# Kernel optimization log

Measured on AMD Instinct MI355X. Metric: run time of the kernel, lower is better.

Reference implementation:

```python
import jax, jax.numpy as jnp
import numpy as np

MUL = 32          # multiplicity of 0e and 1o in node/edge/out irreps
SQRT3 = np.sqrt(3.0).astype(np.float32)


def _split(x, mul):
    # x: [E, mul + mul*3] laid out as [mul x 0e | mul x 1o]
    s = x[:, :mul]
    v = x[:, mul:].reshape(x.shape[0], mul, 3)
    return s, v


def _mlp(x, W1, W2, W3):
    # e3nn-style FullyConnectedNet: no bias, 1/sqrt(fan_in) scaling, silu between layers
    h = jax.nn.silu(x @ (W1 / np.sqrt(np.float32(W1.shape[0]))))
    h = jax.nn.silu(h @ (W2 / np.sqrt(np.float32(W2.shape[0]))))
    return h @ (W3 / np.sqrt(np.float32(W3.shape[0])))


def _tp(s1, v1, s2, v2, W1, W2, W3, W4):
    # 'uvw' tensor product with irreps2 = 1x0e+1x1o (mul2 = 1).
    # CG paths: 0e*0e->0e, 0e*1o->1o, 1o*0e->1o, 1o*1o->0e (dot/sqrt(3)).
    alpha = 1.0 / np.sqrt(np.float32(s1.shape[1]))  # path norm 1/sqrt(mul1*mul2)
    out0a = jnp.einsum('uw,eu->ew', W1, s1 * s2[:, None]) * alpha
    out1a = jnp.einsum('uw,eu,em->ewm', W2, s1, v2) * alpha
    out1b = jnp.einsum('uw,eum->ewm', W3, v1 * s2[:, None, None]) * alpha
    dot = jnp.einsum('eum,em->eu', v1, v2) / SQRT3
    out0b = jnp.einsum('uw,eu->ew', W4, dot) * alpha
    # mid irreps (sorted+simplified): [2*MUL x 0e | 2*MUL x 1o]
    return jnp.concatenate([out0a, out0b], 1), jnp.concatenate([out1a, out1b], 1)


def _lin_scale(ms, mv, w):
    # LinearScaleWithWeights: per-edge generated weights, block per irrep
    E, U = ms.shape
    ws = w[:, :U * MUL].reshape(E, U, MUL)
    wv = w[:, U * MUL:].reshape(E, U, MUL)
    a = 1.0 / np.sqrt(np.float32(U))
    return (jnp.einsum('eu,euw->ew', ms, ws) * a,
            jnp.einsum('eum,euw->ewm', mv, wv) * a)


def _lin_out(s, v, Ls, Lv):
    # o3.Linear with internal shared weights, block-diagonal per irrep
    a = 1.0 / np.sqrt(np.float32(MUL))
    return s @ Ls * a, jnp.einsum('eum,uw->ewm', v, Lv) * a


def reference(node_feats_src, node_feats_dst, edge_feats, local_env_edge, edge_scalars,
              Wn_tp1, Wn_tp2, Wn_tp3, Wn_tp4, We_tp1, We_tp2, We_tp3, We_tp4,
              Wn_mlp1, Wn_mlp2, Wn_mlp3, We_mlp1, We_mlp2, We_mlp3,
              Lns, Lnv, Les, Lev):
    ss, sv = _split(node_feats_src, MUL)
    ds, dv = _split(node_feats_dst, MUL)
    # AttentionHeadsToVector over stacked (src, dst): concat heads along mul axis
    ns = jnp.concatenate([ss, ds], 1)     # [E, 64] (64x0e)
    nv = jnp.concatenate([sv, dv], 1)     # [E, 64, 3] (64x1o)
    es, ev = _split(edge_feats, MUL)
    ls = local_env_edge[:, 0]             # 1x0e
    lv = local_env_edge[:, 1:4]           # 1x1o
    # node branch
    wn = _mlp(edge_scalars, Wn_mlp1, Wn_mlp2, Wn_mlp3)   # [E, 4096]
    ms, mv = _tp(ns, nv, ls, lv, Wn_tp1, Wn_tp2, Wn_tp3, Wn_tp4)
    n_s, n_v = _lin_scale(ms, mv, wn)
    n_s, n_v = _lin_out(n_s, n_v, Lns, Lnv)
    # edge branch
    we = _mlp(edge_scalars, We_mlp1, We_mlp2, We_mlp3)   # [E, 4096]
    ms2, mv2 = _tp(es, ev, ls, lv, We_tp1, We_tp2, We_tp3, We_tp4)
    e_s, e_v = _lin_scale(ms2, mv2, we)
    e_s, e_v = _lin_out(e_s, e_v, Les, Lev)
    out_s = n_s + e_s
    out_v = n_v + e_v
    return jnp.concatenate([out_s, out_v.reshape(out_v.shape[0], -1)], 1)  # [E, 128]


def setup_inputs() -> dict:
    key = jax.random.key(0)
    ks = jax.random.split(key, 23)
    E = 30000
    rn = lambda k, shape: jax.random.normal(k, shape, dtype=jnp.float32)
    return {
        'node_feats_src': rn(ks[0], (E, 128)),
        'node_feats_dst': rn(ks[1], (E, 128)),
        'edge_feats': rn(ks[2], (E, 128)),
        'local_env_edge': rn(ks[3], (E, 4)),
        'edge_scalars': rn(ks[4], (E, 8)),
        'Wn_tp1': rn(ks[5], (64, 32)), 'Wn_tp2': rn(ks[6], (64, 32)),
        'Wn_tp3': rn(ks[7], (64, 32)), 'Wn_tp4': rn(ks[8], (64, 32)),
        'We_tp1': rn(ks[9], (32, 32)), 'We_tp2': rn(ks[10], (32, 32)),
        'We_tp3': rn(ks[11], (32, 32)), 'We_tp4': rn(ks[12], (32, 32)),
        'Wn_mlp1': rn(ks[13], (8, 64)), 'Wn_mlp2': rn(ks[14], (64, 64)),
        'Wn_mlp3': rn(ks[15], (64, 4096)),
        'We_mlp1': rn(ks[16], (8, 64)), 'We_mlp2': rn(ks[17], (64, 64)),
        'We_mlp3': rn(ks[18], (64, 4096)),
        'Lns': rn(ks[19], (32, 32)), 'Lnv': rn(ks[20], (32, 32)),
        'Les': rn(ks[21], (32, 32)), 'Lev': rn(ks[22], (32, 32)),
    }
```

## Files before the change

### kernel.cpp

```cpp
#include <hip/hip_runtime.h>

typedef __attribute__((ext_vector_type(8))) __bf16 bf16x8;
typedef __attribute__((ext_vector_type(4))) float f32x4;

#define MFMA16(A,B,C) __builtin_amdgcn_mfma_f32_16x16x32_bf16(A,B,C,0,0,0)

typedef const __attribute__((address_space(1))) void* gas_ptr;
typedef __attribute__((address_space(3))) void* las_ptr;

#define BARRIER() do { asm volatile("" ::: "memory"); __builtin_amdgcn_s_barrier(); asm volatile("" ::: "memory"); } while (0)
#define WAIT_VM4() asm volatile("s_waitcnt vmcnt(4)" ::: "memory")
#define WAIT_VM0() asm volatile("s_waitcnt vmcnt(0)" ::: "memory")

#define WS_W3N 0
#define WS_W3E 262144
#define WS_TN  524288
#define WS_TE  532480
#define WS_M1N 536576
#define WS_M2N 538624
#define WS_M1E 542720
#define WS_M2E 544768
#define WS_CNT 548864

__global__ void prep_kernel(
    const float* __restrict__ Wn1, const float* __restrict__ Wn2,
    const float* __restrict__ Wn3, const float* __restrict__ Wn4,
    const float* __restrict__ We1, const float* __restrict__ We2,
    const float* __restrict__ We3, const float* __restrict__ We4,
    const float* __restrict__ Mn1, const float* __restrict__ Mn2, const float* __restrict__ Mn3,
    const float* __restrict__ Me1, const float* __restrict__ Me2, const float* __restrict__ Me3,
    const float* __restrict__ Lns, const float* __restrict__ Lnv,
    const float* __restrict__ Les, const float* __restrict__ Lev,
    __bf16* __restrict__ ws)
{
  int idx = blockIdx.x * 256 + threadIdx.x;
  const float c1 = 0.0027621359f;
  const float an = 0.125f;
  const float ae = 0.17677669529663687f;
  const float r3 = 0.5773502691896258f;
  const float m1s = 0.35355339059327373f;
  const float m2s = 0.125f;
  if (idx < 524288) {
    int br = idx >> 18;
    int rem = idx & 262143;
    int j = rem >> 12;
    int kc = rem & 4095;
    int vh = kc >> 11;
    int r2 = kc & 2047;
    int u = r2 >> 5, wp = r2 & 31;
    const float* M3 = br ? Me3 : Mn3;
    const float* L  = vh ? (br ? Lev : Lnv) : (br ? Les : Lns);
    const float* mrow = M3 + (size_t)j * 4096 + vh * 2048 + u * 32;
    float s = 0.f;
    #pragma unroll
    for (int w = 0; w < 32; ++w) s += mrow[w] * L[w * 32 + wp];
    ws[(br ? WS_W3E : WS_W3N) + (size_t)kc * 64 + j] = (__bf16)(s * c1);
  } else if (idx < 524288 + 8192) {
    int t = idx - 524288;
    int i = t >> 11; int r = t & 2047; int w = r >> 6; int u = r & 63;
    const float* W = (i == 0) ? Wn1 : (i == 1) ? Wn2 : (i == 2) ? Wn3 : Wn4;
    float sc = an * ((i == 3) ? r3 : 1.f);
    ws[WS_TN + t] = (__bf16)(W[u * 32 + w] * sc);
  } else if (idx < 524288 + 12288) {
    int t = idx - 532480;
    int i = t >> 10; int r = t & 1023; int w = r >> 5; int u = r & 31;
    const float* W = (i == 0) ? We1 : (i == 1) ? We2 : (i == 2) ? We3 : We4;
    float sc = ae * ((i == 3) ? r3 : 1.f);
    ws[WS_TE + t] = (__bf16)(W[u * 32 + w] * sc);
  } else if (idx < 536576 + 2048) {
    int t = idx - 536576;
    int j = t >> 5, k = t & 31;
    ws[WS_M1N + t] = (__bf16)((k < 8) ? Mn1[k * 64 + j] * m1s : 0.f);
  } else if (idx < 538624 + 4096) {
    int t = idx - 538624;
    int j2 = t >> 6, j = t & 63;
    ws[WS_M2N + t] = (__bf16)(Mn2[j * 64 + j2] * m2s);
  } else if (idx < 542720 + 2048) {
    int t = idx - 542720;
    int j = t >> 5, k = t & 31;
    ws[WS_M1E + t] = (__bf16)((k < 8) ? Me1[k * 64 + j] * m1s : 0.f);
  } else if (idx < 544768 + 4096) {
    int t = idx - 544768;
    int j2 = t >> 6, j = t & 63;
    ws[WS_M2E + t] = (__bf16)(Me2[j * 64 + j2] * m2s);
  }
}

__device__ __forceinline__ float siluf(float x) { return x / (1.0f + __expf(-x)); }
__device__ __forceinline__ unsigned int pk2(float lo, float hi) {
  unsigned short a = __builtin_bit_cast(unsigned short, (__bf16)lo);
  unsigned short b = __builtin_bit_cast(unsigned short, (__bf16)hi);
  return (unsigned int)a | ((unsigned int)b << 16);
}
__device__ __forceinline__ float bflo(unsigned int v) { return __builtin_bit_cast(float, (unsigned int)(v << 16)); }
__device__ __forceinline__ float bfhi(unsigned int v) { return __builtin_bit_cast(float, (unsigned int)(v & 0xffff0000u)); }

__global__ __launch_bounds__(256, 2) void fused_kernel(
    const float* __restrict__ nsrc, const float* __restrict__ ndst,
    const float* __restrict__ efeat, const float* __restrict__ lenv,
    const float* __restrict__ escal,
    const __bf16* __restrict__ ws,
    float* __restrict__ out, int E)
{
  __shared__ __align__(16) char lds[81920];
  const int tid = threadIdx.x;
  const int wave = tid >> 6, l = tid & 63;
  const int lg = l >> 4, li = l & 15;
  const int ebase = blockIdx.x * 64;

  char* coeff = lds;
  char* afpriv = lds + 32768 + wave * 12288;
  char* h2n = lds + 32768;
  char* h2e = lds + 32768 + 8192;

  const int uh  = wave >> 1;
  const int rtw = wave & 1;

  auto stage = [&](int buf, int branch, int b) {
    const char* gbase = (const char*)(ws + (branch ? WS_W3E : WS_W3N));
    int u = uh * 32 + b;
    char* dst = afpriv + buf * 4096 + l * 16;
    int srow = rtw * 16 + (l >> 3);
    int scol = ((l & 7) ^ (l >> 3)) << 4;
    const char* src = gbase + (size_t)u * 4096 + srow * 128 + scol;
    #pragma unroll
    for (int r = 0; r < 4; ++r) {
      int gv = r >> 1, j = r & 1;
      __builtin_amdgcn_global_load_lds((gas_ptr)(src + gv * 262144 + j * 1024),
                                       (las_ptr)(dst + gv * 2048 + j * 1024), 16, 0, 0);
    }
  };

  {
    const int br = wave >> 1;
    const __bf16* M1 = ws + (br ? WS_M1E : WS_M1N);
    const __bf16* M2 = ws + (br ? WS_M2E : WS_M2N);
    char* h2buf = br ? h2e : h2n;
    char* h1s = lds + wave * 8192;
    #pragma unroll 1
    for (int c2 = 0; c2 < 2; ++c2) {
      int ct = (wave & 1) * 2 + c2;
      int el = ct * 16 + li;
      int hl = c2 * 16 + li;
      int ee = min(ebase + el, E - 1);
      bf16x8 bx;
      #pragma unroll
      for (int i = 0; i < 8; ++i) bx[i] = (__bf16)0.f;
      if (lg == 0) {
        const float* xp = escal + (size_t)ee * 8;
        float4 t0 = *(const float4*)(xp);
        float4 t1 = *(const float4*)(xp + 4);
        bx[0]=(__bf16)t0.x; bx[1]=(__bf16)t0.y; bx[2]=(__bf16)t0.z; bx[3]=(__bf16)t0.w;
        bx[4]=(__bf16)t1.x; bx[5]=(__bf16)t1.y; bx[6]=(__bf16)t1.z; bx[7]=(__bf16)t1.w;
      }
      f32x4 hc[4];
      #pragma unroll
      for (int rt = 0; rt < 4; ++rt) {
        bf16x8 a = *(const bf16x8*)(M1 + (rt * 16 + li) * 32 + lg * 8);
        f32x4 c = {0.f, 0.f, 0.f, 0.f};
        hc[rt] = MFMA16(a, bx, c);
      }
      #pragma unroll
      for (int rt = 0; rt < 4; ++rt) {
        int j0 = rt * 16 + lg * 4;
        int g = j0 >> 3;
        int addr = hl * 128 + (((g ^ (hl & 7)) << 4)) + (j0 & 7) * 2;
        uint2 wv; wv.x = pk2(siluf(hc[rt][0]), siluf(hc[rt][1]));
        wv.y = pk2(siluf(hc[rt][2]), siluf(hc[rt][3]));
        *(uint2*)(h1s + addr) = wv;
      }
      f32x4 h2c[4];
      #pragma unroll
      for (int rt = 0; rt < 4; ++rt) { f32x4 z = {0.f,0.f,0.f,0.f}; h2c[rt] = z; }
      #pragma unroll
      for (int kj = 0; kj < 2; ++kj) {
        bf16x8 b = *(const bf16x8*)(h1s + hl * 128 + (((kj * 4 + lg) ^ (hl & 7)) << 4));
        #pragma unroll
        for (int rt = 0; rt < 4; ++rt) {
          bf16x8 a = *(const bf16x8*)(M2 + (rt * 16 + li) * 64 + kj * 32 + lg * 8);
          h2c[rt] = MFMA16(a, b, h2c[rt]);
        }
      }
      #pragma unroll
      for (int rt = 0; rt < 4; ++rt) {
        int j0 = rt * 16 + lg * 4;
        int g = j0 >> 3;
        int addr = el * 128 + (((g ^ (el & 7)) << 4)) + (j0 & 7) * 2;
        uint2 wv; wv.x = pk2(siluf(h2c[rt][0]), siluf(h2c[rt][1]));
        wv.y = pk2(siluf(h2c[rt][2]), siluf(h2c[rt][3]));
        *(uint2*)(h2buf + addr) = wv;
      }
    }
  }
  __syncthreads();

  bf16x8 bbN[4][2], bbE[4][2];
  #pragma unroll
  for (int ct = 0; ct < 4; ++ct)
    #pragma unroll
    for (int kj = 0; kj < 2; ++kj) {
      int el = ct * 16 + li;
      int off = el * 128 + (((kj * 4 + lg) ^ (el & 7)) << 4);
      bbN[ct][kj] = *(const bf16x8*)(h2n + off);
      bbE[ct][kj] = *(const bf16x8*)(h2e + off);
    }
  __syncthreads();

  auto q_phase = [&](const float* f0, const float* f1, int nk, const __bf16* T, int ustride) {
    #pragma unroll 1
    for (int ct = 0; ct < 4; ++ct) {
      int el = ct * 16 + li;
      int ee = min(ebase + el, E - 1);
      const float4 le = *(const float4*)(lenv + (size_t)ee * 4);
      const size_t erow = (size_t)ee * 128;
      if (uh == 0) {
        f32x4 q1c = {0.f,0.f,0.f,0.f}, q2c = {0.f,0.f,0.f,0.f};
        for (int kj = 0; kj < nk; ++kj) {
          const float* fp = (kj ? f1 : f0) + erow + lg * 8;
          float4 t0 = *(const float4*)(fp);
          float4 t1 = *(const float4*)(fp + 4);
          bf16x8 b;
          b[0]=(__bf16)t0.x; b[1]=(__bf16)t0.y; b[2]=(__bf16)t0.z; b[3]=(__bf16)t0.w;
          b[4]=(__bf16)t1.x; b[5]=(__bf16)t1.y; b[6]=(__bf16)t1.z; b[7]=(__bf16)t1.w;
          bf16x8 a1 = *(const bf16x8*)(T + (rtw * 16 + li) * ustride + kj * 32 + lg * 8);
          bf16x8 a2 = *(const bf16x8*)(T + 32 * ustride + (rtw * 16 + li) * ustride + kj * 32 + lg * 8);
          q1c = MFMA16(a1, b, q1c);
          q2c = MFMA16(a2, b, q2c);
        }
        #pragma unroll
        for (int r = 0; r < 4; ++r) {
          uint2 cw;
          cw.x = pk2(q1c[r] * le.x, q2c[r] * le.y);
          cw.y = pk2(q2c[r] * le.z, q2c[r] * le.w);
          *(uint2*)(coeff + (rtw * 16 + lg * 4 + r) * 512 + el * 8) = cw;
        }
      } else {
        f32x4 q30 = {0.f,0.f,0.f,0.f}, q31 = {0.f,0.f,0.f,0.f}, q32 = {0.f,0.f,0.f,0.f}, q4c = {0.f,0.f,0.f,0.f};
        for (int kj = 0; kj < nk; ++kj) {
          const float* fp = (kj ? f1 : f0) + erow + 32 + lg * 24;
          float v[24];
          #pragma unroll
          for (int q = 0; q < 6; ++q) {
            float4 t = *(const float4*)(fp + q * 4);
            v[q*4] = t.x; v[q*4+1] = t.y; v[q*4+2] = t.z; v[q*4+3] = t.w;
          }
          bf16x8 b0, b1, b2, bd;
          #pragma unroll
          for (int i = 0; i < 8; ++i) {
            b0[i] = (__bf16)v[3*i]; b1[i] = (__bf16)v[3*i+1]; b2[i] = (__bf16)v[3*i+2];
            bd[i] = (__bf16)(v[3*i] * le.y + v[3*i+1] * le.z + v[3*i+2] * le.w);
          }
          bf16x8 a3 = *(const bf16x8*)(T + 2 * 32 * ustride + (rtw * 16 + li) * ustride + kj * 32 + lg * 8);
          bf16x8 a4 = *(const bf16x8*)(T + 3 * 32 * ustride + (rtw * 16 + li) * ustride + kj * 32 + lg * 8);
          q30 = MFMA16(a3, b0, q30); q31 = MFMA16(a3, b1, q31); q32 = MFMA16(a3, b2, q32);
          q4c = MFMA16(a4, bd, q4c);
        }
        #pragma unroll
        for (int r = 0; r < 4; ++r) {
          uint2 cw;
          cw.x = pk2(q4c[r], q30[r] * le.x);
          cw.y = pk2(q31[r] * le.x, q32[r] * le.x);
          *(uint2*)(coeff + (32 + rtw * 16 + lg * 4 + r) * 512 + el * 8) = cw;
        }
      }
    }
  };

  f32x4 aS[4], aV[4][3];
  #pragma unroll
  for (int ct = 0; ct < 4; ++ct) {
    f32x4 z = {0.f,0.f,0.f,0.f};
    aS[ct] = z; aV[ct][0] = z; aV[ct][1] = z; aV[ct][2] = z;
  }

  auto main_block = [&](int buf, int b, const bf16x8 (&bb)[4][2]) {
    const char* afb = afpriv + buf * 4096;
    int u_rel = uh * 32 + b;
    bf16x8 afS[2], afV[2];
    #pragma unroll
    for (int kj = 0; kj < 2; ++kj) {
      int off = li * 128 + (((kj * 4 + lg) ^ (li & 7)) << 4);
      afS[kj] = *(const bf16x8*)(afb + off);
      afV[kj] = *(const bf16x8*)(afb + 2048 + off);
    }
    #pragma unroll
    for (int ct = 0; ct < 4; ++ct) {
      uint2 cf = *(const uint2*)(coeff + u_rel * 512 + (ct * 16 + li) * 8);
      float ms = bflo(cf.x), m0 = bfhi(cf.x), m1 = bflo(cf.y), m2 = bfhi(cf.y);
      f32x4 c = {0.f,0.f,0.f,0.f};
      c = MFMA16(afS[0], bb[ct][0], c);
      c = MFMA16(afS[1], bb[ct][1], c);
      aS[ct] += ms * c;
      f32x4 d = {0.f,0.f,0.f,0.f};
      d = MFMA16(afV[0], bb[ct][0], d);
      d = MFMA16(afV[1], bb[ct][1], d);
      aV[ct][0] += m0 * d;
      aV[ct][1] += m1 * d;
      aV[ct][2] += m2 * d;
    }
  };

  stage(0, 0, 0);
  stage(1, 0, 1);
  q_phase(nsrc, ndst, 2, ws + WS_TN, 64);
  __syncthreads();

  #pragma unroll 1
  for (int b = 0; b < 32; ++b) {
    if (b < 30) stage((b + 2) % 3, 0, b + 2);
    else        stage((b + 2) % 3, 1, b - 30);
    main_block(b % 3, b, bbN);
    WAIT_VM4();
  }
  BARRIER();

  q_phase(efeat, efeat, 1, ws + WS_TE, 32);
  __syncthreads();

  #pragma unroll 1
  for (int b = 0; b < 32; ++b) {
    if (b < 30) stage((b + 4) % 3, 1, b + 2);
    main_block((b + 2) % 3, b, bbE);
    if (b == 30) { WAIT_VM0(); }
    else         { WAIT_VM4(); }
  }
  BARRIER();

  char* R1 = lds;
  auto rmw = [&](bool add) {
    #pragma unroll
    for (int ct = 0; ct < 4; ++ct) {
      int e = ct * 16 + li;
      char* epp = R1 + e * 512;
      f32x4 s = aS[ct];
      char* p = epp + (((rtw * 4 + lg) ^ (e & 7)) << 4);
      if (add) s += *(const f32x4*)p;
      *(f32x4*)p = s;
      #pragma unroll
      for (int m = 0; m < 3; ++m) {
        f32x4 x = aV[ct][m];
        char* q = epp + (((8 + m * 8 + rtw * 4 + lg) ^ (e & 7)) << 4);
        if (add) x += *(const f32x4*)q;
        *(f32x4*)q = x;
      }
    }
  };
  if (uh == 0) rmw(false);
  __syncthreads();
  if (uh == 1) rmw(true);
  __syncthreads();

  #pragma unroll
  for (int it = 0; it < 8; ++it) {
    int chunk = it * 256 + tid;
    int e = chunk >> 5, c4 = chunk & 31;
    f32x4 v;
    #pragma unroll
    for (int q = 0; q < 4; ++q) {
      int f = c4 * 4 + q;
      int g, wd;
      if (f < 32) { g = f >> 2; wd = f & 3; }
      else { int t = f - 32; int w = t / 3; int m = t - w * 3; g = 8 + m * 8 + (w >> 2); wd = w & 3; }
      v[q] = *(const float*)(R1 + e * 512 + ((g ^ (e & 7)) << 4) + wd * 4);
    }
    int ge = ebase + e;
    if (ge < E) *(f32x4*)(out + (size_t)ge * 128 + c4 * 4) = v;
  }
}

extern "C" void kernel_launch(void* const* d_in, const int* in_sizes, int n_in,
                              void* d_out, int out_size, void* d_ws, size_t ws_size,
                              hipStream_t stream) {
  const float* nsrc  = (const float*)d_in[0];
  const float* ndst  = (const float*)d_in[1];
  const float* efeat = (const float*)d_in[2];
  const float* lenv  = (const float*)d_in[3];
  const float* escal = (const float*)d_in[4];
  const float* Wn1 = (const float*)d_in[5];
  const float* Wn2 = (const float*)d_in[6];
  const float* Wn3 = (const float*)d_in[7];
  const float* Wn4 = (const float*)d_in[8];
  const float* We1 = (const float*)d_in[9];
  const float* We2 = (const float*)d_in[10];
  const float* We3 = (const float*)d_in[11];
  const float* We4 = (const float*)d_in[12];
  const float* Mn1 = (const float*)d_in[13];
  const float* Mn2 = (const float*)d_in[14];
  const float* Mn3 = (const float*)d_in[15];
  const float* Me1 = (const float*)d_in[16];
  const float* Me2 = (const float*)d_in[17];
  const float* Me3 = (const float*)d_in[18];
  const float* Lns = (const float*)d_in[19];
  const float* Lnv = (const float*)d_in[20];
  const float* Les = (const float*)d_in[21];
  const float* Lev = (const float*)d_in[22];
  (void)n_in; (void)ws_size;

  int E = in_sizes[0] / 128;
  __bf16* ws = (__bf16*)d_ws;
  float* outp = (float*)d_out;
  (void)out_size;

  int nprep = (WS_CNT + 255) / 256;
  hipLaunchKernelGGL(prep_kernel, dim3(nprep), dim3(256), 0, stream,
                     Wn1, Wn2, Wn3, Wn4, We1, We2, We3, We4,
                     Mn1, Mn2, Mn3, Me1, Me2, Me3,
                     Lns, Lnv, Les, Lev, ws);

  int nwg = (E + 63) / 64;
  hipLaunchKernelGGL(fused_kernel, dim3(nwg), dim3(256), 0, stream,
                     nsrc, ndst, efeat, lenv, escal, ws, outp, E);
}
```

Before: 75.95 us.

## Split node and edge branches into separate workgroups combined by atomic adds

```diff
diff --git a/kernel.cpp b/kernel.cpp
--- a/kernel.cpp
+++ b/kernel.cpp
@@ -9,7 +9,6 @@
 typedef __attribute__((address_space(3))) void* las_ptr;
 
 #define BARRIER() do { asm volatile("" ::: "memory"); __builtin_amdgcn_s_barrier(); asm volatile("" ::: "memory"); } while (0)
-#define WAIT_VM4() asm volatile("s_waitcnt vmcnt(4)" ::: "memory")
 #define WAIT_VM0() asm volatile("s_waitcnt vmcnt(0)" ::: "memory")
 
 #define WS_W3N 0
@@ -102,107 +101,100 @@
     const __bf16* __restrict__ ws,
     float* __restrict__ out, int E)
 {
-  __shared__ __align__(16) char lds[81920];
+  __shared__ __align__(16) char lds[57344];
   const int tid = threadIdx.x;
   const int wave = tid >> 6, l = tid & 63;
   const int lg = l >> 4, li = l & 15;
-  const int ebase = blockIdx.x * 64;
+  const int br = blockIdx.x & 1;
+  const int ebase = (blockIdx.x >> 1) * 64;
 
   char* coeff = lds;
-  char* afpriv = lds + 32768 + wave * 12288;
-  char* h2n = lds + 32768;
-  char* h2e = lds + 32768 + 8192;
-
-  const int uh  = wave >> 1;
+  char* afbase = lds + 32768;
+  char* h2buf = afbase;
+
+  const int ep  = wave >> 1;
   const int rtw = wave & 1;
-
-  auto stage = [&](int buf, int branch, int b) {
-    const char* gbase = (const char*)(ws + (branch ? WS_W3E : WS_W3N));
-    int u = uh * 32 + b;
-    char* dst = afpriv + buf * 4096 + l * 16;
-    int srow = rtw * 16 + (l >> 3);
-    int scol = ((l & 7) ^ (l >> 3)) << 4;
-    const char* src = gbase + (size_t)u * 4096 + srow * 128 + scol;
-    #pragma unroll
-    for (int r = 0; r < 4; ++r) {
-      int gv = r >> 1, j = r & 1;
-      __builtin_amdgcn_global_load_lds((gas_ptr)(src + gv * 262144 + j * 1024),
-                                       (las_ptr)(dst + gv * 2048 + j * 1024), 16, 0, 0);
+  const int qh  = wave >> 1;
+  const int qr  = wave & 1;
+
+  const char* gbase = (const char*)(ws + (br ? WS_W3E : WS_W3N));
+
+  auto stage = [&](int buf, int u) {
+    int row = tid >> 3, col = tid & 7;
+    int roff = row * 128 + (((col ^ (row & 7))) << 4);
+    char* dst = afbase + buf * 8192 + tid * 16;
+    #pragma unroll
+    for (int r = 0; r < 2; ++r) {
+      const char* src = gbase + r * 262144 + (size_t)u * 4096 + roff;
+      __builtin_amdgcn_global_load_lds((gas_ptr)src, (las_ptr)(dst + r * 4096), 16, 0, 0);
     }
   };
 
   {
-    const int br = wave >> 1;
     const __bf16* M1 = ws + (br ? WS_M1E : WS_M1N);
     const __bf16* M2 = ws + (br ? WS_M2E : WS_M2N);
-    char* h2buf = br ? h2e : h2n;
     char* h1s = lds + wave * 8192;
-    #pragma unroll 1
-    for (int c2 = 0; c2 < 2; ++c2) {
-      int ct = (wave & 1) * 2 + c2;
-      int el = ct * 16 + li;
-      int hl = c2 * 16 + li;
-      int ee = min(ebase + el, E - 1);
-      bf16x8 bx;
-      #pragma unroll
-      for (int i = 0; i < 8; ++i) bx[i] = (__bf16)0.f;
-      if (lg == 0) {
-        const float* xp = escal + (size_t)ee * 8;
-        float4 t0 = *(const float4*)(xp);
-        float4 t1 = *(const float4*)(xp + 4);
-        bx[0]=(__bf16)t0.x; bx[1]=(__bf16)t0.y; bx[2]=(__bf16)t0.z; bx[3]=(__bf16)t0.w;
-        bx[4]=(__bf16)t1.x; bx[5]=(__bf16)t1.y; bx[6]=(__bf16)t1.z; bx[7]=(__bf16)t1.w;
-      }
-      f32x4 hc[4];
+    int el = wave * 16 + li;
+    int hl = li;
+    int ee = min(ebase + el, E - 1);
+    bf16x8 bx;
+    #pragma unroll
+    for (int i = 0; i < 8; ++i) bx[i] = (__bf16)0.f;
+    if (lg == 0) {
+      const float* xp = escal + (size_t)ee * 8;
+      float4 t0 = *(const float4*)(xp);
+      float4 t1 = *(const float4*)(xp + 4);
+      bx[0]=(__bf16)t0.x; bx[1]=(__bf16)t0.y; bx[2]=(__bf16)t0.z; bx[3]=(__bf16)t0.w;
+      bx[4]=(__bf16)t1.x; bx[5]=(__bf16)t1.y; bx[6]=(__bf16)t1.z; bx[7]=(__bf16)t1.w;
+    }
+    f32x4 hc[4];
+    #pragma unroll
+    for (int rt = 0; rt < 4; ++rt) {
+      bf16x8 a = *(const bf16x8*)(M1 + (rt * 16 + li) * 32 + lg * 8);
+      f32x4 c = {0.f, 0.f, 0.f, 0.f};
+      hc[rt] = MFMA16(a, bx, c);
+    }
+    #pragma unroll
+    for (int rt = 0; rt < 4; ++rt) {
+      int j0 = rt * 16 + lg * 4;
+      int g = j0 >> 3;
+      int addr = hl * 128 + (((g ^ (hl & 7)) << 4)) + (j0 & 7) * 2;
+      uint2 wv; wv.x = pk2(siluf(hc[rt][0]), siluf(hc[rt][1]));
+      wv.y = pk2(siluf(hc[rt][2]), siluf(hc[rt][3]));
+      *(uint2*)(h1s + addr) = wv;
+    }
+    f32x4 h2c[4];
+    #pragma unroll
+    for (int rt = 0; rt < 4; ++rt) { f32x4 z = {0.f,0.f,0.f,0.f}; h2c[rt] = z; }
+    #pragma unroll
+    for (int kj = 0; kj < 2; ++kj) {
+      bf16x8 b = *(const bf16x8*)(h1s + hl * 128 + (((kj * 4 + lg) ^ (hl & 7)) << 4));
       #pragma unroll
       for (int rt = 0; rt < 4; ++rt) {
-        bf16x8 a = *(const bf16x8*)(M1 + (rt * 16 + li) * 32 + lg * 8);
-        f32x4 c = {0.f, 0.f, 0.f, 0.f};
-        hc[rt] = MFMA16(a, bx, c);
+        bf16x8 a = *(const bf16x8*)(M2 + (rt * 16 + li) * 64 + kj * 32 + lg * 8);
+        h2c[rt] = MFMA16(a, b, h2c[rt]);
       }
-      #pragma unroll
-      for (int rt = 0; rt < 4; ++rt) {
-        int j0 = rt * 16 + lg * 4;
-        int g = j0 >> 3;
-        int addr = hl * 128 + (((g ^ (hl & 7)) << 4)) + (j0 & 7) * 2;
-        uint2 wv; wv.x = pk2(siluf(hc[rt][0]), siluf(hc[rt][1]));
-        wv.y = pk2(siluf(hc[rt][2]), siluf(hc[rt][3]));
-        *(uint2*)(h1s + addr) = wv;
-      }
-      f32x4 h2c[4];
-      #pragma unroll
-      for (int rt = 0; rt < 4; ++rt) { f32x4 z = {0.f,0.f,0.f,0.f}; h2c[rt] = z; }
-      #pragma unroll
-      for (int kj = 0; kj < 2; ++kj) {
-        bf16x8 b = *(const bf16x8*)(h1s + hl * 128 + (((kj * 4 + lg) ^ (hl & 7)) << 4));
-        #pragma unroll
-        for (int rt = 0; rt < 4; ++rt) {
-          bf16x8 a = *(const bf16x8*)(M2 + (rt * 16 + li) * 64 + kj * 32 + lg * 8);
-          h2c[rt] = MFMA16(a, b, h2c[rt]);
-        }
-      }
-      #pragma unroll
-      for (int rt = 0; rt < 4; ++rt) {
-        int j0 = rt * 16 + lg * 4;
-        int g = j0 >> 3;
-        int addr = el * 128 + (((g ^ (el & 7)) << 4)) + (j0 & 7) * 2;
-        uint2 wv; wv.x = pk2(siluf(h2c[rt][0]), siluf(h2c[rt][1]));
-        wv.y = pk2(siluf(h2c[rt][2]), siluf(h2c[rt][3]));
-        *(uint2*)(h2buf + addr) = wv;
-      }
+    }
+    #pragma unroll
+    for (int rt = 0; rt < 4; ++rt) {
+      int j0 = rt * 16 + lg * 4;
+      int g = j0 >> 3;
+      int addr = el * 128 + (((g ^ (el & 7)) << 4)) + (j0 & 7) * 2;
+      uint2 wv; wv.x = pk2(siluf(h2c[rt][0]), siluf(h2c[rt][1]));
+      wv.y = pk2(siluf(h2c[rt][2]), siluf(h2c[rt][3]));
+      *(uint2*)(h2buf + addr) = wv;
     }
   }
   __syncthreads();
 
-  bf16x8 bbN[4][2], bbE[4][2];
+  bf16x8 bb[2][2];
   #pragma unroll
-  for (int ct = 0; ct < 4; ++ct)
+  for (int ct2 = 0; ct2 < 2; ++ct2)
     #pragma unroll
     for (int kj = 0; kj < 2; ++kj) {
-      int el = ct * 16 + li;
+      int el = ep * 32 + ct2 * 16 + li;
       int off = el * 128 + (((kj * 4 + lg) ^ (el & 7)) << 4);
-      bbN[ct][kj] = *(const bf16x8*)(h2n + off);
-      bbE[ct][kj] = *(const bf16x8*)(h2e + off);
+      bb[ct2][kj] = *(const bf16x8*)(h2buf + off);
     }
   __syncthreads();
 
@@ -213,7 +205,7 @@
       int ee = min(ebase + el, E - 1);
       const float4 le = *(const float4*)(lenv + (size_t)ee * 4);
       const size_t erow = (size_t)ee * 128;
-      if (uh == 0) {
+      if (qh == 0) {
         f32x4 q1c = {0.f,0.f,0.f,0.f}, q2c = {0.f,0.f,0.f,0.f};
         for (int kj = 0; kj < nk; ++kj) {
           const float* fp = (kj ? f1 : f0) + erow + lg * 8;
@@ -222,8 +214,8 @@
           bf16x8 b;
           b[0]=(__bf16)t0.x; b[1]=(__bf16)t0.y; b[2]=(__bf16)t0.z; b[3]=(__bf16)t0.w;
           b[4]=(__bf16)t1.x; b[5]=(__bf16)t1.y; b[6]=(__bf16)t1.z; b[7]=(__bf16)t1.w;
-          bf16x8 a1 = *(const bf16x8*)(T + (rtw * 16 + li) * ustride + kj * 32 + lg * 8);
-          bf16x8 a2 = *(const bf16x8*)(T + 32 * ustride + (rtw * 16 + li) * ustride + kj * 32 + lg * 8);
+          bf16x8 a1 = *(const bf16x8*)(T + (qr * 16 + li) * ustride + kj * 32 + lg * 8);
+          bf16x8 a2 = *(const bf16x8*)(T + 32 * ustride + (qr * 16 + li) * ustride + kj * 32 + lg * 8);
           q1c = MFMA16(a1, b, q1c);
           q2c = MFMA16(a2, b, q2c);
         }
@@ -232,7 +224,7 @@
           uint2 cw;
           cw.x = pk2(q1c[r] * le.x, q2c[r] * le.y);
           cw.y = pk2(q2c[r] * le.z, q2c[r] * le.w);
-          *(uint2*)(coeff + (rtw * 16 + lg * 4 + r) * 512 + el * 8) = cw;
+          *(uint2*)(coeff + (qr * 16 + lg * 4 + r) * 512 + el * 8) = cw;
         }
       } else {
         f32x4 q30 = {0.f,0.f,0.f,0.f}, q31 = {0.f,0.f,0.f,0.f}, q32 = {0.f,0.f,0.f,0.f}, q4c = {0.f,0.f,0.f,0.f};
@@ -250,8 +242,8 @@
             b0[i] = (__bf16)v[3*i]; b1[i] = (__bf16)v[3*i+1]; b2[i] = (__bf16)v[3*i+2];
             bd[i] = (__bf16)(v[3*i] * le.y + v[3*i+1] * le.z + v[3*i+2] * le.w);
           }
-          bf16x8 a3 = *(const bf16x8*)(T + 2 * 32 * ustride + (rtw * 16 + li) * ustride + kj * 32 + lg * 8);
-          bf16x8 a4 = *(const bf16x8*)(T + 3 * 32 * ustride + (rtw * 16 + li) * ustride + kj * 32 + lg * 8);
+          bf16x8 a3 = *(const bf16x8*)(T + 2 * 32 * ustride + (qr * 16 + li) * ustride + kj * 32 + lg * 8);
+          bf16x8 a4 = *(const bf16x8*)(T + 3 * 32 * ustride + (qr * 16 + li) * ustride + kj * 32 + lg * 8);
           q30 = MFMA16(a3, b0, q30); q31 = MFMA16(a3, b1, q31); q32 = MFMA16(a3, b2, q32);
           q4c = MFMA16(a4, bd, q4c);
         }
@@ -260,94 +252,71 @@
           uint2 cw;
           cw.x = pk2(q4c[r], q30[r] * le.x);
           cw.y = pk2(q31[r] * le.x, q32[r] * le.x);
-          *(uint2*)(coeff + (32 + rtw * 16 + lg * 4 + r) * 512 + el * 8) = cw;
+          *(uint2*)(coeff + (32 + qr * 16 + lg * 4 + r) * 512 + el * 8) = cw;
         }
       }
     }
   };
 
-  f32x4 aS[4], aV[4][3];
+  f32x4 aS[2], aV[2][3];
   #pragma unroll
-  for (int ct = 0; ct < 4; ++ct) {
+  for (int ct2 = 0; ct2 < 2; ++ct2) {
     f32x4 z = {0.f,0.f,0.f,0.f};
-    aS[ct] = z; aV[ct][0] = z; aV[ct][1] = z; aV[ct][2] = z;
-  }
-
-  auto main_block = [&](int buf, int b, const bf16x8 (&bb)[4][2]) {
-    const char* afb = afpriv + buf * 4096;
-    int u_rel = uh * 32 + b;
+    aS[ct2] = z; aV[ct2][0] = z; aV[ct2][1] = z; aV[ct2][2] = z;
+  }
+
+  auto main_block = [&](int buf, int u) {
+    const char* afb = afbase + buf * 8192;
     bf16x8 afS[2], afV[2];
     #pragma unroll
     for (int kj = 0; kj < 2; ++kj) {
-      int off = li * 128 + (((kj * 4 + lg) ^ (li & 7)) << 4);
+      int off = (rtw * 16 + li) * 128 + (((kj * 4 + lg) ^ (li & 7)) << 4);
       afS[kj] = *(const bf16x8*)(afb + off);
-      afV[kj] = *(const bf16x8*)(afb + 2048 + off);
-    }
-    #pragma unroll
-    for (int ct = 0; ct < 4; ++ct) {
-      uint2 cf = *(const uint2*)(coeff + u_rel * 512 + (ct * 16 + li) * 8);
+      afV[kj] = *(const bf16x8*)(afb + 4096 + off);
+    }
+    #pragma unroll
+    for (int ct2 = 0; ct2 < 2; ++ct2) {
+      int e = ep * 32 + ct2 * 16 + li;
+      uint2 cf = *(const uint2*)(coeff + u * 512 + e * 8);
       float ms = bflo(cf.x), m0 = bfhi(cf.x), m1 = bflo(cf.y), m2 = bfhi(cf.y);
       f32x4 c = {0.f,0.f,0.f,0.f};
-      c = MFMA16(afS[0], bb[ct][0], c);
-      c = MFMA16(afS[1], bb[ct][1], c);
-      aS[ct] += ms * c;
+      c = MFMA16(afS[0], bb[ct2][0], c);
+      c = MFMA16(afS[1], bb[ct2][1], c);
+      aS[ct2] += ms * c;
       f32x4 d = {0.f,0.f,0.f,0.f};
-      d = MFMA16(afV[0], bb[ct][0], d);
-      d = MFMA16(afV[1], bb[ct][1], d);
-      aV[ct][0] += m0 * d;
-      aV[ct][1] += m1 * d;
-      aV[ct][2] += m2 * d;
+      d = MFMA16(afV[0], bb[ct2][0], d);
+      d = MFMA16(afV[1], bb[ct2][1], d);
+      aV[ct2][0] += m0 * d;
+      aV[ct2][1] += m1 * d;
+      aV[ct2][2] += m2 * d;
     }
   };
 
-  stage(0, 0, 0);
-  stage(1, 0, 1);
-  q_phase(nsrc, ndst, 2, ws + WS_TN, 64);
+  stage(0, 0);
+  stage(1, 1);
+  if (br == 0) q_phase(nsrc, ndst, 2, ws + WS_TN, 64);
+  else         q_phase(efeat, efeat, 1, ws + WS_TE, 32);
   __syncthreads();
 
   #pragma unroll 1
-  for (int b = 0; b < 32; ++b) {
-    if (b < 30) stage((b + 2) % 3, 0, b + 2);
-    else        stage((b + 2) % 3, 1, b - 30);
-    main_block(b % 3, b, bbN);
-    WAIT_VM4();
-  }
-  BARRIER();
-
-  q_phase(efeat, efeat, 1, ws + WS_TE, 32);
-  __syncthreads();
-
-  #pragma unroll 1
-  for (int b = 0; b < 32; ++b) {
-    if (b < 30) stage((b + 4) % 3, 1, b + 2);
-    main_block((b + 2) % 3, b, bbE);
-    if (b == 30) { WAIT_VM0(); }
-    else         { WAIT_VM4(); }
-  }
-  BARRIER();
+  for (int b = 0; b < 64; ++b) {
+    if (b < 62) stage((b + 2) % 3, b + 2);
+    main_block(b % 3, b);
+    WAIT_VM0();
+    BARRIER();
+  }
 
   char* R1 = lds;
-  auto rmw = [&](bool add) {
-    #pragma unroll
-    for (int ct = 0; ct < 4; ++ct) {
-      int e = ct * 16 + li;
-      char* epp = R1 + e * 512;
-      f32x4 s = aS[ct];
-      char* p = epp + (((rtw * 4 + lg) ^ (e & 7)) << 4);
-      if (add) s += *(const f32x4*)p;
-      *(f32x4*)p = s;
-      #pragma unroll
-      for (int m = 0; m < 3; ++m) {
-        f32x4 x = aV[ct][m];
-        char* q = epp + (((8 + m * 8 + rtw * 4 + lg) ^ (e & 7)) << 4);
-        if (add) x += *(const f32x4*)q;
-        *(f32x4*)q = x;
-      }
-    }
-  };
-  if (uh == 0) rmw(false);
-  __syncthreads();
-  if (uh == 1) rmw(true);
+  #pragma unroll
+  for (int ct2 = 0; ct2 < 2; ++ct2) {
+    int e = ep * 32 + ct2 * 16 + li;
+    char* epp = R1 + e * 512;
+    f32x4 s = aS[ct2];
+    *(f32x4*)(epp + (((rtw * 4 + lg) ^ (e & 7)) << 4)) = s;
+    #pragma unroll
+    for (int m = 0; m < 3; ++m)
+      *(f32x4*)(epp + (((8 + m * 8 + rtw * 4 + lg) ^ (e & 7)) << 4)) = aV[ct2][m];
+  }
   __syncthreads();
 
   #pragma unroll
@@ -364,7 +333,13 @@
       v[q] = *(const float*)(R1 + e * 512 + ((g ^ (e & 7)) << 4) + wd * 4);
     }
     int ge = ebase + e;
-    if (ge < E) *(f32x4*)(out + (size_t)ge * 128 + c4 * 4) = v;
+    if (ge < E) {
+      float* dst = out + (size_t)ge * 128 + c4 * 4;
+      atomicAdd(dst + 0, v[0]);
+      atomicAdd(dst + 1, v[1]);
+      atomicAdd(dst + 2, v[2]);
+      atomicAdd(dst + 3, v[3]);
+    }
   }
 }
 
@@ -399,7 +374,8 @@
   int E = in_sizes[0] / 128;
   __bf16* ws = (__bf16*)d_ws;
   float* outp = (float*)d_out;
-  (void)out_size;
+
+  hipMemsetAsync(d_out, 0, (size_t)out_size * sizeof(float), stream);
 
   int nprep = (WS_CNT + 255) / 256;
   hipLaunchKernelGGL(prep_kernel, dim3(nprep), dim3(256), 0, stream,
@@ -407,7 +383,7 @@
                      Mn1, Mn2, Mn3, Me1, Me2, Me3,
                      Lns, Lnv, Les, Lev, ws);
 
-  int nwg = (E + 63) / 64;
-  hipLaunchKernelGGL(fused_kernel, dim3(nwg), dim3(256), 0, stream,
+  int ngroups = (E + 63) / 64;
+  hipLaunchKernelGGL(fused_kernel, dim3(ngroups * 2), dim3(256), 0, stream,
                      nsrc, ndst, efeat, lenv, escal, ws, outp, E);
 }
```

Measured after the change: 172.6 us. 127% more time.

## Halve edges per block, share staged weights across waves, double-buffer with barriers

Applied to the files above, without the earlier changes.

```diff
diff --git a/kernel.cpp b/kernel.cpp
--- a/kernel.cpp
+++ b/kernel.cpp
@@ -7,10 +7,6 @@
 
 typedef const __attribute__((address_space(1))) void* gas_ptr;
 typedef __attribute__((address_space(3))) void* las_ptr;
-
-#define BARRIER() do { asm volatile("" ::: "memory"); __builtin_amdgcn_s_barrier(); asm volatile("" ::: "memory"); } while (0)
-#define WAIT_VM4() asm volatile("s_waitcnt vmcnt(4)" ::: "memory")
-#define WAIT_VM0() asm volatile("s_waitcnt vmcnt(0)" ::: "memory")
 
 #define WS_W3N 0
 #define WS_W3E 262144
@@ -95,120 +91,115 @@
 __device__ __forceinline__ float bflo(unsigned int v) { return __builtin_bit_cast(float, (unsigned int)(v << 16)); }
 __device__ __forceinline__ float bfhi(unsigned int v) { return __builtin_bit_cast(float, (unsigned int)(v & 0xffff0000u)); }
 
-__global__ __launch_bounds__(256, 2) void fused_kernel(
+__global__ __launch_bounds__(256, 3) void fused_kernel(
     const float* __restrict__ nsrc, const float* __restrict__ ndst,
     const float* __restrict__ efeat, const float* __restrict__ lenv,
     const float* __restrict__ escal,
     const __bf16* __restrict__ ws,
     float* __restrict__ out, int E)
 {
-  __shared__ __align__(16) char lds[81920];
+  __shared__ __align__(16) char lds[49152];
   const int tid = threadIdx.x;
   const int wave = tid >> 6, l = tid & 63;
   const int lg = l >> 4, li = l & 15;
-  const int ebase = blockIdx.x * 64;
+  const int ebase = blockIdx.x * 32;
 
   char* coeff = lds;
-  char* afpriv = lds + 32768 + wave * 12288;
-  char* h2n = lds + 32768;
-  char* h2e = lds + 32768 + 8192;
+  char* afbase = lds + 16384;
+  char* h2n = afbase;
+  char* h2e = afbase + 4096;
 
   const int uh  = wave >> 1;
   const int rtw = wave & 1;
 
   auto stage = [&](int buf, int branch, int b) {
     const char* gbase = (const char*)(ws + (branch ? WS_W3E : WS_W3N));
-    int u = uh * 32 + b;
-    char* dst = afpriv + buf * 4096 + l * 16;
-    int srow = rtw * 16 + (l >> 3);
-    int scol = ((l & 7) ^ (l >> 3)) << 4;
-    const char* src = gbase + (size_t)u * 4096 + srow * 128 + scol;
+    char* dst = afbase + buf * 16384 + tid * 16;
+    int row = tid >> 3, col = tid & 7;
+    int roff = row * 128 + ((col ^ (row & 7)) << 4);
     #pragma unroll
     for (int r = 0; r < 4; ++r) {
-      int gv = r >> 1, j = r & 1;
-      __builtin_amdgcn_global_load_lds((gas_ptr)(src + gv * 262144 + j * 1024),
-                                       (las_ptr)(dst + gv * 2048 + j * 1024), 16, 0, 0);
+      int u = b + (r >> 1) * 32, gv = r & 1;
+      const char* src = gbase + gv * 262144 + u * 4096 + roff;
+      __builtin_amdgcn_global_load_lds((gas_ptr)src, (las_ptr)(dst + r * 4096), 16, 0, 0);
     }
   };
 
   {
     const int br = wave >> 1;
+    const int ct = wave & 1;
     const __bf16* M1 = ws + (br ? WS_M1E : WS_M1N);
     const __bf16* M2 = ws + (br ? WS_M2E : WS_M2N);
     char* h2buf = br ? h2e : h2n;
-    char* h1s = lds + wave * 8192;
-    #pragma unroll 1
-    for (int c2 = 0; c2 < 2; ++c2) {
-      int ct = (wave & 1) * 2 + c2;
-      int el = ct * 16 + li;
-      int hl = c2 * 16 + li;
-      int ee = min(ebase + el, E - 1);
-      bf16x8 bx;
-      #pragma unroll
-      for (int i = 0; i < 8; ++i) bx[i] = (__bf16)0.f;
-      if (lg == 0) {
-        const float* xp = escal + (size_t)ee * 8;
-        float4 t0 = *(const float4*)(xp);
-        float4 t1 = *(const float4*)(xp + 4);
-        bx[0]=(__bf16)t0.x; bx[1]=(__bf16)t0.y; bx[2]=(__bf16)t0.z; bx[3]=(__bf16)t0.w;
-        bx[4]=(__bf16)t1.x; bx[5]=(__bf16)t1.y; bx[6]=(__bf16)t1.z; bx[7]=(__bf16)t1.w;
-      }
-      f32x4 hc[4];
+    char* h1s = lds + wave * 4096;
+    int el = ct * 16 + li;
+    int hl = li;
+    int ee = min(ebase + el, E - 1);
+    bf16x8 bx;
+    #pragma unroll
+    for (int i = 0; i < 8; ++i) bx[i] = (__bf16)0.f;
+    if (lg == 0) {
+      const float* xp = escal + (size_t)ee * 8;
+      float4 t0 = *(const float4*)(xp);
+      float4 t1 = *(const float4*)(xp + 4);
+      bx[0]=(__bf16)t0.x; bx[1]=(__bf16)t0.y; bx[2]=(__bf16)t0.z; bx[3]=(__bf16)t0.w;
+      bx[4]=(__bf16)t1.x; bx[5]=(__bf16)t1.y; bx[6]=(__bf16)t1.z; bx[7]=(__bf16)t1.w;
+    }
+    f32x4 hc[4];
+    #pragma unroll
+    for (int rt = 0; rt < 4; ++rt) {
+      bf16x8 a = *(const bf16x8*)(M1 + (rt * 16 + li) * 32 + lg * 8);
+      f32x4 c = {0.f, 0.f, 0.f, 0.f};
+      hc[rt] = MFMA16(a, bx, c);
+    }
+    #pragma unroll
+    for (int rt = 0; rt < 4; ++rt) {
+      int j0 = rt * 16 + lg * 4;
+      int g = j0 >> 3;
+      int addr = hl * 128 + (((g ^ (hl & 7)) << 4)) + (j0 & 7) * 2;
+      uint2 wv; wv.x = pk2(siluf(hc[rt][0]), siluf(hc[rt][1]));
+      wv.y = pk2(siluf(hc[rt][2]), siluf(hc[rt][3]));
+      *(uint2*)(h1s + addr) = wv;
+    }
+    f32x4 h2c[4];
+    #pragma unroll
+    for (int rt = 0; rt < 4; ++rt) { f32x4 z = {0.f,0.f,0.f,0.f}; h2c[rt] = z; }
+    #pragma unroll
+    for (int kj = 0; kj < 2; ++kj) {
+      bf16x8 b = *(const bf16x8*)(h1s + hl * 128 + (((kj * 4 + lg) ^ (hl & 7)) << 4));
       #pragma unroll
       for (int rt = 0; rt < 4; ++rt) {
-        bf16x8 a = *(const bf16x8*)(M1 + (rt * 16 + li) * 32 + lg * 8);
-        f32x4 c = {0.f, 0.f, 0.f, 0.f};
-        hc[rt] = MFMA16(a, bx, c);
+        bf16x8 a = *(const bf16x8*)(M2 + (rt * 16 + li) * 64 + kj * 32 + lg * 8);
+        h2c[rt] = MFMA16(a, b, h2c[rt]);
       }
-      #pragma unroll
-      for (int rt = 0; rt < 4; ++rt) {
-        int j0 = rt * 16 + lg * 4;
-        int g = j0 >> 3;
-        int addr = hl * 128 + (((g ^ (hl & 7)) << 4)) + (j0 & 7) * 2;
-        uint2 wv; wv.x = pk2(siluf(hc[rt][0]), siluf(hc[rt][1]));
-        wv.y = pk2(siluf(hc[rt][2]), siluf(hc[rt][3]));
-        *(uint2*)(h1s + addr) = wv;
-      }
-      f32x4 h2c[4];
-      #pragma unroll
-      for (int rt = 0; rt < 4; ++rt) { f32x4 z = {0.f,0.f,0.f,0.f}; h2c[rt] = z; }
-      #pragma unroll
-      for (int kj = 0; kj < 2; ++kj) {
-        bf16x8 b = *(const bf16x8*)(h1s + hl * 128 + (((kj * 4 + lg) ^ (hl & 7)) << 4));
-        #pragma unroll
-        for (int rt = 0; rt < 4; ++rt) {
-          bf16x8 a = *(const bf16x8*)(M2 + (rt * 16 + li) * 64 + kj * 32 + lg * 8);
-          h2c[rt] = MFMA16(a, b, h2c[rt]);
-        }
-      }
-      #pragma unroll
-      for (int rt = 0; rt < 4; ++rt) {
-        int j0 = rt * 16 + lg * 4;
-        int g = j0 >> 3;
-        int addr = el * 128 + (((g ^ (el & 7)) << 4)) + (j0 & 7) * 2;
-        uint2 wv; wv.x = pk2(siluf(h2c[rt][0]), siluf(h2c[rt][1]));
-        wv.y = pk2(siluf(h2c[rt][2]), siluf(h2c[rt][3]));
-        *(uint2*)(h2buf + addr) = wv;
-      }
-    }
-  }
-  __syncthreads();
-
-  bf16x8 bbN[4][2], bbE[4][2];
+    }
+    #pragma unroll
+    for (int rt = 0; rt < 4; ++rt) {
+      int j0 = rt * 16 + lg * 4;
+      int g = j0 >> 3;
+      int addr = el * 128 + (((g ^ (el & 7)) << 4)) + (j0 & 7) * 2;
+      uint2 wv; wv.x = pk2(siluf(h2c[rt][0]), siluf(h2c[rt][1]));
+      wv.y = pk2(siluf(h2c[rt][2]), siluf(h2c[rt][3]));
+      *(uint2*)(h2buf + addr) = wv;
+    }
+  }
+  __syncthreads();
+
+  bf16x8 bbN[2][2], bbE[2][2];
   #pragma unroll
-  for (int ct = 0; ct < 4; ++ct)
+  for (int ct2 = 0; ct2 < 2; ++ct2)
     #pragma unroll
     for (int kj = 0; kj < 2; ++kj) {
-      int el = ct * 16 + li;
+      int el = ct2 * 16 + li;
       int off = el * 128 + (((kj * 4 + lg) ^ (el & 7)) << 4);
-      bbN[ct][kj] = *(const bf16x8*)(h2n + off);
-      bbE[ct][kj] = *(const bf16x8*)(h2e + off);
+      bbN[ct2][kj] = *(const bf16x8*)(h2n + off);
+      bbE[ct2][kj] = *(const bf16x8*)(h2e + off);
     }
   __syncthreads();
 
   auto q_phase = [&](const float* f0, const float* f1, int nk, const __bf16* T, int ustride) {
     #pragma unroll 1
-    for (int ct = 0; ct < 4; ++ct) {
+    for (int ct = 0; ct < 2; ++ct) {
       int el = ct * 16 + li;
       int ee = min(ebase + el, E - 1);
       const float4 le = *(const float4*)(lenv + (size_t)ee * 4);
@@ -232,7 +223,7 @@
           uint2 cw;
           cw.x = pk2(q1c[r] * le.x, q2c[r] * le.y);
           cw.y = pk2(q2c[r] * le.z, q2c[r] * le.w);
-          *(uint2*)(coeff + (rtw * 16 + lg * 4 + r) * 512 + el * 8) = cw;
+          *(uint2*)(coeff + (rtw * 16 + lg * 4 + r) * 256 + el * 8) = cw;
         }
       } else {
         f32x4 q30 = {0.f,0.f,0.f,0.f}, q31 = {0.f,0.f,0.f,0.f}, q32 = {0.f,0.f,0.f,0.f}, q4c = {0.f,0.f,0.f,0.f};
@@ -260,85 +251,82 @@
           uint2 cw;
           cw.x = pk2(q4c[r], q30[r] * le.x);
           cw.y = pk2(q31[r] * le.x, q32[r] * le.x);
-          *(uint2*)(coeff + (32 + rtw * 16 + lg * 4 + r) * 512 + el * 8) = cw;
+          *(uint2*)(coeff + (32 + rtw * 16 + lg * 4 + r) * 256 + el * 8) = cw;
         }
       }
     }
   };
 
-  f32x4 aS[4], aV[4][3];
+  f32x4 aS[2], aV[2][3];
   #pragma unroll
-  for (int ct = 0; ct < 4; ++ct) {
+  for (int ct2 = 0; ct2 < 2; ++ct2) {
     f32x4 z = {0.f,0.f,0.f,0.f};
-    aS[ct] = z; aV[ct][0] = z; aV[ct][1] = z; aV[ct][2] = z;
-  }
-
-  auto main_block = [&](int buf, int b, const bf16x8 (&bb)[4][2]) {
-    const char* afb = afpriv + buf * 4096;
-    int u_rel = uh * 32 + b;
+    aS[ct2] = z; aV[ct2][0] = z; aV[ct2][1] = z; aV[ct2][2] = z;
+  }
+
+  auto main_block = [&](int buf, int b, const bf16x8 (&bb)[2][2]) {
+    const char* afb = afbase + buf * 16384 + uh * 8192;
+    int u = uh * 32 + b;
     bf16x8 afS[2], afV[2];
     #pragma unroll
     for (int kj = 0; kj < 2; ++kj) {
-      int off = li * 128 + (((kj * 4 + lg) ^ (li & 7)) << 4);
+      int off = (rtw * 16 + li) * 128 + (((kj * 4 + lg) ^ (li & 7)) << 4);
       afS[kj] = *(const bf16x8*)(afb + off);
-      afV[kj] = *(const bf16x8*)(afb + 2048 + off);
-    }
-    #pragma unroll
-    for (int ct = 0; ct < 4; ++ct) {
-      uint2 cf = *(const uint2*)(coeff + u_rel * 512 + (ct * 16 + li) * 8);
+      afV[kj] = *(const bf16x8*)(afb + 4096 + off);
+    }
+    #pragma unroll
+    for (int ct2 = 0; ct2 < 2; ++ct2) {
+      int e = ct2 * 16 + li;
+      uint2 cf = *(const uint2*)(coeff + u * 256 + e * 8);
       float ms = bflo(cf.x), m0 = bfhi(cf.x), m1 = bflo(cf.y), m2 = bfhi(cf.y);
       f32x4 c = {0.f,0.f,0.f,0.f};
-      c = MFMA16(afS[0], bb[ct][0], c);
-      c = MFMA16(afS[1], bb[ct][1], c);
-      aS[ct] += ms * c;
+      c = MFMA16(afS[0], bb[ct2][0], c);
+      c = MFMA16(afS[1], bb[ct2][1], c);
+      aS[ct2] += ms * c;
       f32x4 d = {0.f,0.f,0.f,0.f};
-      d = MFMA16(afV[0], bb[ct][0], d);
-      d = MFMA16(afV[1], bb[ct][1], d);
-      aV[ct][0] += m0 * d;
-      aV[ct][1] += m1 * d;
-      aV[ct][2] += m2 * d;
+      d = MFMA16(afV[0], bb[ct2][0], d);
+      d = MFMA16(afV[1], bb[ct2][1], d);
+      aV[ct2][0] += m0 * d;
+      aV[ct2][1] += m1 * d;
+      aV[ct2][2] += m2 * d;
     }
   };
 
   stage(0, 0, 0);
-  stage(1, 0, 1);
   q_phase(nsrc, ndst, 2, ws + WS_TN, 64);
   __syncthreads();
 
   #pragma unroll 1
   for (int b = 0; b < 32; ++b) {
-    if (b < 30) stage((b + 2) % 3, 0, b + 2);
-    else        stage((b + 2) % 3, 1, b - 30);
-    main_block(b % 3, b, bbN);
-    WAIT_VM4();
-  }
-  BARRIER();
+    if (b < 31) stage((b + 1) & 1, 0, b + 1);
+    else        stage(0, 1, 0);
+    main_block(b & 1, b, bbN);
+    __syncthreads();
+  }
 
   q_phase(efeat, efeat, 1, ws + WS_TE, 32);
   __syncthreads();
 
   #pragma unroll 1
   for (int b = 0; b < 32; ++b) {
-    if (b < 30) stage((b + 4) % 3, 1, b + 2);
-    main_block((b + 2) % 3, b, bbE);
-    if (b == 30) { WAIT_VM0(); }
-    else         { WAIT_VM4(); }
-  }
-  BARRIER();
+    if (b < 31) stage((b + 1) & 1, 1, b + 1);
+    main_block(b & 1, b, bbE);
+    __syncthreads();
+  }
 
   char* R1 = lds;
   auto rmw = [&](bool add) {
     #pragma unroll
-    for (int ct = 0; ct < 4; ++ct) {
-      int e = ct * 16 + li;
+    for (int ct2 = 0; ct2 < 2; ++ct2) {
+      int e = ct2 * 16 + li;
       char* epp = R1 + e * 512;
-      f32x4 s = aS[ct];
+      f32x4 s = aS[ct2];
       char* p = epp + (((rtw * 4 + lg) ^ (e & 7)) << 4);
       if (add) s += *(const f32x4*)p;
       *(f32x4*)p = s;
       #pragma unroll
       for (int m = 0; m < 3; ++m) {
-        f32x4 x = aV[ct][m];
+        f32x4 x = aV[ct2][m];
         char* q = epp + (((8 + m * 8 + rtw * 4 + lg) ^ (e & 7)) << 4);
         if (add) x += *(const f32x4*)q;
         *(f32x4*)q = x;
@@ -351,7 +339,7 @@
   __syncthreads();
 
   #pragma unroll
-  for (int it = 0; it < 8; ++it) {
+  for (int it = 0; it < 4; ++it) {
     int chunk = it * 256 + tid;
     int e = chunk >> 5, c4 = chunk & 31;
     f32x4 v;
@@ -407,7 +395,7 @@
                      Mn1, Mn2, Mn3, Me1, Me2, Me3,
                      Lns, Lnv, Les, Lev, ws);
 
-  int nwg = (E + 63) / 64;
+  int nwg = (E + 31) / 32;
   hipLaunchKernelGGL(fused_kernel, dim3(nwg), dim3(256), 0, stream,
                      nsrc, ndst, efeat, lenv, escal, ws, outp, E);
 }
```

Result: slower. 103.5 us (+36.3%).
